# Optimization experiments

Hardware: AMD Instinct MI355X
Metric: run time of the kernel (lower is better)

The kernel has to match this reference:

```python
import jax, jax.numpy as jnp
import numpy as np

B = 16384
D1 = 256
D2 = 256
D_FF = 1024
N_BINS = 16
TAIL = 3.0
MIN_VAL = 1e-3
MIN_TOTAL = N_BINS * MIN_VAL
TAIL_CONST = float(np.log(np.exp(1.0 - MIN_VAL) - 1.0))
D_OUT = (3 * N_BINS - 1) * D2  # 12032


def setup_inputs() -> dict:
    key = jax.random.key(0)
    ks = jax.random.split(key, 8)
    s = lambda fan: 1.0 / np.sqrt(fan)
    return {
        'x1': jax.random.normal(ks[0], (B, D1), jnp.float32),
        'x2': jax.random.normal(ks[1], (B, D2), jnp.float32),
        'W0': jax.random.normal(ks[2], (D1, D_FF), jnp.float32) * s(D1),
        'b0': jnp.zeros((D_FF,), jnp.float32),
        'W1': jax.random.normal(ks[3], (D_FF, D_FF), jnp.float32) * s(D_FF),
        'b1': jnp.zeros((D_FF,), jnp.float32),
        'W2': jax.random.normal(ks[4], (D_FF, D_OUT), jnp.float32) * s(D_FF),
        'b2': jnp.zeros((D_OUT,), jnp.float32),
    }


def _rqs_forward(x, wu, hu, du):
    # x: [B, D2]; wu, hu: [B, D2, N_BINS]; du: [B, D2, N_BINS-1]
    widths = MIN_VAL + (1.0 - MIN_TOTAL) * jax.nn.softmax(wu, axis=-1)
    heights = MIN_VAL + (1.0 - MIN_TOTAL) * jax.nn.softmax(hu, axis=-1)
    cw = jnp.cumsum(widths, axis=-1)
    cw = jnp.concatenate([jnp.zeros_like(cw[..., :1]), cw], axis=-1)
    cw = 2.0 * TAIL * cw - TAIL  # x bin edges in [-TAIL, TAIL], [B,D2,N_BINS+1]
    ch = jnp.cumsum(heights, axis=-1)
    ch = jnp.concatenate([jnp.zeros_like(ch[..., :1]), ch], axis=-1)
    ch = 2.0 * TAIL * ch - TAIL  # y bin edges
    w = cw[..., 1:] - cw[..., :-1]
    h = ch[..., 1:] - ch[..., :-1]
    # boundary derivatives padded so softplus(TAIL_CONST)+MIN_VAL == 1 (linear tails)
    pad = jnp.full_like(du[..., :1], TAIL_CONST)
    d = MIN_VAL + jax.nn.softplus(jnp.concatenate([pad, du, pad], axis=-1))  # [B,D2,N_BINS+1]
    inside = (x > -TAIL) & (x < TAIL)
    xc = jnp.clip(x, -TAIL, TAIL)
    # data-dependent bin search against interior edges
    idx = jnp.sum((xc[..., None] >= cw[..., 1:-1]).astype(jnp.int32), axis=-1)  # [B,D2]
    take = lambda a: jnp.take_along_axis(a, idx[..., None], axis=-1)[..., 0]
    xk = take(cw[..., :-1]); yk = take(ch[..., :-1])
    wk = take(w); hk = take(h)
    dk = take(d[..., :-1]); dk1 = take(d[..., 1:])
    sk = hk / wk
    theta = (xc - xk) / wk
    t1m = theta * (1.0 - theta)
    denom = sk + (dk + dk1 - 2.0 * sk) * t1m
    y = yk + hk * (sk * theta * theta + dk * t1m) / denom
    deriv = sk * sk * (dk1 * theta * theta + 2.0 * sk * t1m + dk * (1.0 - theta) ** 2) / (denom * denom)
    y = jnp.where(inside, y, x)            # identity tails
    logdet = jnp.where(inside, jnp.log(deriv), 0.0)
    return y, jnp.sum(logdet, axis=-1)     # [B,D2], [B]


def reference(x1, x2, W0, b0, W1, b1, W2, b2):
    # conditioner MLP: x1 -> spline parameters
    hdn = jax.nn.relu(x1 @ W0 + b0)
    hdn = jax.nn.relu(hdn @ W1 + b1)
    p = (hdn @ W2 + b2).reshape(-1, D2, 3 * N_BINS - 1)
    wu = p[..., :N_BINS]
    hu = p[..., N_BINS:2 * N_BINS]
    du = p[..., 2 * N_BINS:]
    y2, logdet = _rqs_forward(x2, wu, hu, du)
    return y2, logdet
```

## Files before the change

### kernel.cpp

```cpp
#include <hip/hip_runtime.h>
#include <math.h>

using u16 = unsigned short;
using bf16x8 = __attribute__((ext_vector_type(8))) short;
using f32x4  = __attribute__((ext_vector_type(4))) float;

#define DEV static __device__ __forceinline__

DEV u16 f2bf(float f) {
  union { float f; unsigned u; } v; v.f = f;
  unsigned u = v.u + 0x7fffu + ((v.u >> 16) & 1u);
  return (u16)(u >> 16);
}

DEV void gload16(const void* g, void* l) {
  __builtin_amdgcn_global_load_lds(
      (const __attribute__((address_space(1))) void*)g,
      (__attribute__((address_space(3))) void*)l, 16, 0, 0);
}

__global__ void k_conv_bf16(const float* __restrict__ in, u16* __restrict__ out, int n) {
  int i = blockIdx.x * 256 + threadIdx.x;
  if (i < n) out[i] = f2bf(in[i]);
}

__global__ void k_transconv(const float* __restrict__ in, u16* __restrict__ out,
                            int K, int Nin, int Nout, int pack) {
  __shared__ float t[32][33];
  int kb = blockIdx.x * 32, nb = blockIdx.y * 32;
  int tx = threadIdx.x & 31, ty = threadIdx.x >> 5;
  #pragma unroll
  for (int i = 0; i < 4; ++i) {
    int k = kb + ty + i * 8;
    int no = nb + tx;
    float v = 0.f;
    if (k < K && no < Nout) {
      if (pack) {
        int r = no % 48;
        if (r < 47) v = in[(size_t)k * Nin + (no / 48) * 47 + r];
      } else {
        v = in[(size_t)k * Nin + no];
      }
    }
    t[ty + i * 8][tx] = v;
  }
  __syncthreads();
  #pragma unroll
  for (int i = 0; i < 4; ++i) {
    int no = nb + ty + i * 8;
    int k = kb + tx;
    if (no < Nout && k < K) out[(size_t)no * K + k] = f2bf(t[tx][ty + i * 8]);
  }
}

__global__ __launch_bounds__(256)
void k_gemm_relu(const u16* __restrict__ A, const u16* __restrict__ Bt,
                 const float* __restrict__ bias, u16* __restrict__ C,
                 int N, int K) {
  constexpr int BM = 128, BN = 128, BK = 32;
  __shared__ __align__(16) u16 lds[(BM + BN) * BK];
  int tid = threadIdx.x, w = tid >> 6, lane = tid & 63;
  int bn = blockIdx.x, bm = blockIdx.y;
  int brow = bm * BM, bcol = bn * BN;
  int wm = w >> 1, wn = w & 1;
  int fr = lane & 15, fg = lane >> 4;
  f32x4 acc[4][4];
  #pragma unroll
  for (int i = 0; i < 4; ++i)
    #pragma unroll
    for (int j = 0; j < 4; ++j) acc[i][j] = (f32x4){0.f, 0.f, 0.f, 0.f};

  constexpr int ACH = BM * BK / 8;
  constexpr int CALLS = (BM + BN) * BK / 8 / 64;

  for (int kt = 0; kt < K; kt += BK) {
    for (int j = 0; j * 4 + w < CALLS; ++j) {
      int cb = (j * 4 + w) * 64;
      int c = cb + lane;
      const u16* g;
      if (c < ACH) {
        int row = c >> 2, c8 = c & 3;
        g = A + (size_t)(brow + row) * K + kt + c8 * 8;
      } else {
        int b = c - ACH;
        int nn = b >> 2, c8 = b & 3;
        g = Bt + (size_t)(bcol + nn) * K + kt + c8 * 8;
      }
      gload16(g, &lds[cb * 8]);
    }
    asm volatile("s_waitcnt vmcnt(0)" ::: "memory");
    __syncthreads();

    const u16* Al = lds;
    const u16* Bl = lds + BM * BK;
    bf16x8 af[4], bfr[4];
    #pragma unroll
    for (int mi = 0; mi < 4; ++mi)
      af[mi] = *(const bf16x8*)&Al[(wm * 64 + mi * 16 + fr) * BK + fg * 8];
    #pragma unroll
    for (int ni = 0; ni < 4; ++ni)
      bfr[ni] = *(const bf16x8*)&Bl[(wn * 64 + ni * 16 + fr) * BK + fg * 8];
    #pragma unroll
    for (int mi = 0; mi < 4; ++mi)
      #pragma unroll
      for (int ni = 0; ni < 4; ++ni)
        acc[mi][ni] = __builtin_amdgcn_mfma_f32_16x16x32_bf16(af[mi], bfr[ni], acc[mi][ni], 0, 0, 0);
    __syncthreads();
  }

  #pragma unroll
  for (int ni = 0; ni < 4; ++ni) {
    int col = bcol + wn * 64 + ni * 16 + fr;
    float bb = bias[col];
    #pragma unroll
    for (int mi = 0; mi < 4; ++mi) {
      #pragma unroll
      for (int q = 0; q < 4; ++q) {
        int row = brow + wm * 64 + mi * 16 + fg * 4 + q;
        float vv = acc[mi][ni][q] + bb;
        C[(size_t)row * N + col] = f2bf(vv > 0.f ? vv : 0.f);
      }
    }
  }
}

__global__ __launch_bounds__(256, 2)
void k_gemm3_fused(const u16* __restrict__ A, const u16* __restrict__ Bt,
                   const float* __restrict__ b2, const float* __restrict__ x2,
                   float* __restrict__ y2, float* __restrict__ ldpart) {
  extern __shared__ char smem[];
  const int tid = threadIdx.x, w = tid >> 6, lane = tid & 63;
  const int fr = lane & 15, fg = lane >> 4;

  const int bid = blockIdx.x;
  const int bm = bid >> 6;
  const int bn = ((bid & 7) << 3) | ((bid >> 3) & 7);
  const int brow = bm * 256;

  const int csrc = (tid & 7) ^ ((tid >> 3) & 7);
  const u16* gB[6];
  #pragma unroll
  for (int k = 0; k < 6; ++k)
    gB[k] = Bt + (size_t)(bn * 192 + (tid >> 3) + 32 * k) * 1024 + csrc * 8;

#define ISSUE_B(t1) {                                                 \
    const size_t ko_ = (size_t)(t1) * 64;                             \
    char* pb_ = smem + ((t1) & 1) * 24576;                            \
    gload16(gB[0] + ko_, pb_ + tid * 16);                             \
    gload16(gB[1] + ko_, pb_ + tid * 16 + 4096);                      \
    gload16(gB[2] + ko_, pb_ + tid * 16 + 8192);                      \
    gload16(gB[3] + ko_, pb_ + tid * 16 + 12288);                     \
    gload16(gB[4] + ko_, pb_ + tid * 16 + 16384);                     \
    gload16(gB[5] + ko_, pb_ + tid * 16 + 20480); }

  const u16* gAm[4];
  #pragma unroll
  for (int m = 0; m < 4; ++m)
    gAm[m] = A + (size_t)(brow + w * 64 + m * 16 + fr) * 1024 + fg * 8;

  const int sc0 = ((fg ^ (fr & 7)) << 4);
  const int sc1 = (((4 + fg) ^ (fr & 7)) << 4);

  f32x4 acc[4][12];
  #pragma unroll
  for (int m = 0; m < 4; ++m)
    #pragma unroll
    for (int n = 0; n < 12; ++n) acc[m][n] = (f32x4){0.f, 0.f, 0.f, 0.f};

  bf16x8 a[4][2];

  ISSUE_B(0);
  #pragma unroll
  for (int m = 0; m < 4; ++m) {
    a[m][0] = *(const bf16x8*)(gAm[m]);
    a[m][1] = *(const bf16x8*)(gAm[m] + 32);
  }
  asm volatile("s_waitcnt vmcnt(0)" ::: "memory");
  __syncthreads();

  for (int t = 0; t < 16; ++t) {
    if (t < 15) ISSUE_B(t + 1);
    const char* Bb = smem + (t & 1) * 24576;
    __builtin_amdgcn_s_setprio(1);
    #pragma unroll
    for (int kk = 0; kk < 2; ++kk) {
      const int sc = kk ? sc1 : sc0;
      #pragma unroll
      for (int n = 0; n < 12; ++n) {
        bf16x8 b = *(const bf16x8*)(Bb + (n * 16 + fr) * 128 + sc);
        #pragma unroll
        for (int m = 0; m < 4; ++m)
          acc[m][n] = __builtin_amdgcn_mfma_f32_16x16x32_bf16(a[m][kk], b, acc[m][n], 0, 0, 0);
      }
    }
    __builtin_amdgcn_s_setprio(0);
    if (t < 15) {
      const size_t ko = (size_t)(t + 1) * 64;
      #pragma unroll
      for (int m = 0; m < 4; ++m) {
        a[m][0] = *(const bf16x8*)(gAm[m] + ko);
        a[m][1] = *(const bf16x8*)(gAm[m] + ko + 32);
      }
      asm volatile("s_waitcnt vmcnt(0)" ::: "memory");
      __syncthreads();
    }
  }
  __syncthreads();

  float* slot = (float*)smem;
  float* ldacc = (float*)(smem + 50176);
  #pragma unroll
  for (int g = 0; g < 4; ++g) {
    #pragma unroll
    for (int m = 0; m < 4; ++m)
      #pragma unroll
      for (int j = 0; j < 3; ++j) {
        const int n = g * 3 + j;
        #pragma unroll
        for (int q = 0; q < 4; ++q)
          slot[(w * 64 + m * 16 + fg * 4 + q) * 49 + j * 16 + fr] = acc[m][n][q];
      }
    __syncthreads();
    {
      const int r = tid;
      const float* pr = slot + r * 49;
      const int grow = brow + r;
      const int d2 = bn * 4 + g;
      const float* bb = b2 + (size_t)d2 * 47;

      float wv[16], hv[16];
      #pragma unroll
      for (int j = 0; j < 16; ++j) wv[j] = pr[j] + bb[j];
      #pragma unroll
      for (int j = 0; j < 16; ++j) hv[j] = pr[16 + j] + bb[16 + j];

      float x = x2[(size_t)grow * 256 + d2];
      float xc = fminf(fmaxf(x, -3.f), 3.f);

      float mw = wv[0];
      #pragma unroll
      for (int j = 1; j < 16; ++j) mw = fmaxf(mw, wv[j]);
      float sw = 0.f;
      #pragma unroll
      for (int j = 0; j < 16; ++j) { wv[j] = __expf(wv[j] - mw); sw += wv[j]; }
      float scw = 0.984f / sw;

      float mh = hv[0];
      #pragma unroll
      for (int j = 1; j < 16; ++j) mh = fmaxf(mh, hv[j]);
      float sh = 0.f;
      #pragma unroll
      for (int j = 0; j < 16; ++j) { hv[j] = __expf(hv[j] - mh); sh += hv[j]; }
      float sch = 0.984f / sh;

      int idx = 0;
      float xk = -3.f, cum = 0.f;
      #pragma unroll
      for (int i = 1; i <= 15; ++i) {
        cum += 0.001f + wv[i - 1] * scw;
        float cwi = 6.f * cum - 3.f;
        if (xc >= cwi) { idx = i; xk = cwi; }
      }
      float yk = -3.f, cumh = 0.f;
      #pragma unroll
      for (int i = 1; i <= 15; ++i) {
        cumh += 0.001f + hv[i - 1] * sch;
        float chi = 6.f * cumh - 3.f;
        if (i == idx) yk = chi;
      }
      float wk = 1.f, hk = 1.f;
      #pragma unroll
      for (int i = 0; i < 16; ++i) {
        if (i == idx) {
          wk = 6.f * (0.001f + wv[i] * scw);
          hk = 6.f * (0.001f + hv[i] * sch);
        }
      }
      float dk = 1.f, dk1 = 1.f;
      #pragma unroll
      for (int i = 1; i <= 15; ++i) {
        float u = pr[32 + i - 1] + bb[32 + i - 1];
        float e = __expf(u);
        float dd = 0.001f + (u > 15.f ? u : log1pf(e));
        if (i == idx) dk = dd;
        if (i == idx + 1) dk1 = dd;
      }

      float sk = hk / wk;
      float th = (xc - xk) / wk;
      float om = 1.f - th;
      float t1m = th * om;
      float den = sk + (dk + dk1 - 2.f * sk) * t1m;
      float y = yk + hk * (sk * th * th + dk * t1m) / den;
      float deriv = sk * sk * (dk1 * th * th + 2.f * sk * t1m + dk * om * om) / (den * den);
      bool inside = (x > -3.f) && (x < 3.f);
      float yout = inside ? y : x;
      float ld = inside ? __logf(deriv) : 0.f;

      y2[(size_t)grow * 256 + d2] = yout;
      ldacc[r * 4 + g] = ld;
    }
    __syncthreads();
  }

  {
    float s = ldacc[tid * 4] + ldacc[tid * 4 + 1] + ldacc[tid * 4 + 2] + ldacc[tid * 4 + 3];
    ldpart[(size_t)bn * 16384 + brow + tid] = s;
  }
}

__global__ void k_reduce_ld(const float* __restrict__ part, float* __restrict__ out) {
  int r = blockIdx.x * 256 + threadIdx.x;
  float s = 0.f;
  for (int j = 0; j < 64; ++j) s += part[(size_t)j * 16384 + r];
  out[r] = s;
}

extern "C" void kernel_launch(void* const* d_in, const int* in_sizes, int n_in,
                              void* d_out, int out_size, void* d_ws, size_t ws_size,
                              hipStream_t stream) {
  const float* x1 = (const float*)d_in[0];
  const float* x2 = (const float*)d_in[1];
  const float* W0 = (const float*)d_in[2];
  const float* b0 = (const float*)d_in[3];
  const float* W1 = (const float*)d_in[4];
  const float* b1 = (const float*)d_in[5];
  const float* W2 = (const float*)d_in[6];
  const float* b2 = (const float*)d_in[7];
  float* y2 = (float*)d_out;
  float* logdet = y2 + (size_t)16384 * 256;

  char* ws = (char*)d_ws;
  u16* W2t = (u16*)ws;
  u16* W0t = (u16*)(ws + 25165824);
  u16* W1t = (u16*)(ws + 25165824 + 524288);
  u16* x1b = (u16*)(ws + 27787264);
  float* ldp = (float*)(ws + 27787264);
  u16* h1  = (u16*)(ws + 36175872);
  u16* h2  = (u16*)(ws + 69730304);

  hipFuncSetAttribute((const void*)k_gemm3_fused,
                      hipFuncAttributeMaxDynamicSharedMemorySize, 54272);

  k_conv_bf16<<<16384, 256, 0, stream>>>(x1, x1b, 16384 * 256);
  k_transconv<<<dim3(8, 32), 256, 0, stream>>>(W0, W0t, 256, 1024, 1024, 0);
  k_transconv<<<dim3(32, 32), 256, 0, stream>>>(W1, W1t, 1024, 1024, 1024, 0);
  k_transconv<<<dim3(32, 384), 256, 0, stream>>>(W2, W2t, 1024, 12032, 12288, 1);

  k_gemm_relu<<<dim3(8, 128), 256, 0, stream>>>(x1b, W0t, b0, h1, 1024, 256);
  k_gemm_relu<<<dim3(8, 128), 256, 0, stream>>>(h1, W1t, b1, h2, 1024, 1024);
  k_gemm3_fused<<<4096, 256, 54272, stream>>>(h2, W2t, b2, x2, y2, ldp);
  k_reduce_ld<<<64, 256, 0, stream>>>(ldp, logdet);
}
```

Measured before the change: 752.4 us.

## Halve gemm3 row tile to raise occupancy and split A-load waits

The fused final GEMM now uses a 128-row tile instead of 256, which halves the accumulator registers per thread and doubles the grid. Launch bounds go up to 4 blocks per CU and shared memory drops slightly. The k-loop is split into two half-steps so the A-fragment reloads overlap the MFMAs, with a partial vmcnt wait and a bare barrier replacing the full wait plus syncthreads. The epilogue processes two d2 columns per pass and writes twice as many logdet partials, which the reduce kernel now sums over 128 slices. The cost is that each B tile is reused across fewer rows, so global and LDS traffic for B roughly doubles.

Measured after the change: 741.8 us. No clear change (-1.4%).

```diff
diff --git a/kernel.cpp b/kernel.cpp
--- a/kernel.cpp
+++ b/kernel.cpp
@@ -124,7 +124,7 @@
   }
 }
 
-__global__ __launch_bounds__(256, 2)
+__global__ __launch_bounds__(256, 4)
 void k_gemm3_fused(const u16* __restrict__ A, const u16* __restrict__ Bt,
                    const float* __restrict__ b2, const float* __restrict__ x2,
                    float* __restrict__ y2, float* __restrict__ ldpart) {
@@ -135,97 +135,95 @@
   const int bid = blockIdx.x;
   const int bm = bid >> 6;
   const int bn = ((bid & 7) << 3) | ((bid >> 3) & 7);
-  const int brow = bm * 256;
+  const int brow = bm * 128;
 
   const int csrc = (tid & 7) ^ ((tid >> 3) & 7);
-  const u16* gB[6];
-  #pragma unroll
-  for (int k = 0; k < 6; ++k)
-    gB[k] = Bt + (size_t)(bn * 192 + (tid >> 3) + 32 * k) * 1024 + csrc * 8;
+  const u16* gB0 = Bt + (size_t)(bn * 192 + (tid >> 3)) * 1024 + csrc * 8;
 
 #define ISSUE_B(t1) {                                                 \
     const size_t ko_ = (size_t)(t1) * 64;                             \
-    char* pb_ = smem + ((t1) & 1) * 24576;                            \
-    gload16(gB[0] + ko_, pb_ + tid * 16);                             \
-    gload16(gB[1] + ko_, pb_ + tid * 16 + 4096);                      \
-    gload16(gB[2] + ko_, pb_ + tid * 16 + 8192);                      \
-    gload16(gB[3] + ko_, pb_ + tid * 16 + 12288);                     \
-    gload16(gB[4] + ko_, pb_ + tid * 16 + 16384);                     \
-    gload16(gB[5] + ko_, pb_ + tid * 16 + 20480); }
-
-  const u16* gAm[4];
-  #pragma unroll
-  for (int m = 0; m < 4; ++m)
-    gAm[m] = A + (size_t)(brow + w * 64 + m * 16 + fr) * 1024 + fg * 8;
+    char* pb_ = smem + ((t1) & 1) * 24576 + tid * 16;                 \
+    gload16(gB0 + ko_, pb_);                                          \
+    gload16(gB0 + 32768 + ko_, pb_ + 4096);                           \
+    gload16(gB0 + 65536 + ko_, pb_ + 8192);                           \
+    gload16(gB0 + 98304 + ko_, pb_ + 12288);                          \
+    gload16(gB0 + 131072 + ko_, pb_ + 16384);                         \
+    gload16(gB0 + 163840 + ko_, pb_ + 20480); }
+
+  const u16* gA0 = A + (size_t)(brow + w * 32 + fr) * 1024 + fg * 8;
 
   const int sc0 = ((fg ^ (fr & 7)) << 4);
   const int sc1 = (((4 + fg) ^ (fr & 7)) << 4);
 
-  f32x4 acc[4][12];
-  #pragma unroll
-  for (int m = 0; m < 4; ++m)
+  f32x4 acc[2][12];
+  #pragma unroll
+  for (int m = 0; m < 2; ++m)
     #pragma unroll
     for (int n = 0; n < 12; ++n) acc[m][n] = (f32x4){0.f, 0.f, 0.f, 0.f};
 
-  bf16x8 a[4][2];
+  bf16x8 a[2][2];
 
   ISSUE_B(0);
-  #pragma unroll
-  for (int m = 0; m < 4; ++m) {
-    a[m][0] = *(const bf16x8*)(gAm[m]);
-    a[m][1] = *(const bf16x8*)(gAm[m] + 32);
-  }
+  a[0][0] = *(const bf16x8*)(gA0);
+  a[0][1] = *(const bf16x8*)(gA0 + 32);
+  a[1][0] = *(const bf16x8*)(gA0 + 16384);
+  a[1][1] = *(const bf16x8*)(gA0 + 16384 + 32);
   asm volatile("s_waitcnt vmcnt(0)" ::: "memory");
   __syncthreads();
 
   for (int t = 0; t < 16; ++t) {
     if (t < 15) ISSUE_B(t + 1);
     const char* Bb = smem + (t & 1) * 24576;
+    const size_t ko = (size_t)(t + 1) * 64;
     __builtin_amdgcn_s_setprio(1);
     #pragma unroll
-    for (int kk = 0; kk < 2; ++kk) {
-      const int sc = kk ? sc1 : sc0;
-      #pragma unroll
-      for (int n = 0; n < 12; ++n) {
-        bf16x8 b = *(const bf16x8*)(Bb + (n * 16 + fr) * 128 + sc);
-        #pragma unroll
-        for (int m = 0; m < 4; ++m)
-          acc[m][n] = __builtin_amdgcn_mfma_f32_16x16x32_bf16(a[m][kk], b, acc[m][n], 0, 0, 0);
-      }
+    for (int n = 0; n < 12; ++n) {
+      bf16x8 b = *(const bf16x8*)(Bb + (n * 16 + fr) * 128 + sc0);
+      acc[0][n] = __builtin_amdgcn_mfma_f32_16x16x32_bf16(a[0][0], b, acc[0][n], 0, 0, 0);
+      acc[1][n] = __builtin_amdgcn_mfma_f32_16x16x32_bf16(a[1][0], b, acc[1][n], 0, 0, 0);
     }
     __builtin_amdgcn_s_setprio(0);
     if (t < 15) {
-      const size_t ko = (size_t)(t + 1) * 64;
-      #pragma unroll
-      for (int m = 0; m < 4; ++m) {
-        a[m][0] = *(const bf16x8*)(gAm[m] + ko);
-        a[m][1] = *(const bf16x8*)(gAm[m] + ko + 32);
-      }
-      asm volatile("s_waitcnt vmcnt(0)" ::: "memory");
-      __syncthreads();
-    }
-  }
-  __syncthreads();
-
-  float* slot = (float*)smem;
-  float* ldacc = (float*)(smem + 50176);
-  #pragma unroll
-  for (int g = 0; g < 4; ++g) {
-    #pragma unroll
-    for (int m = 0; m < 4; ++m)
-      #pragma unroll
-      for (int j = 0; j < 3; ++j) {
-        const int n = g * 3 + j;
+      a[0][0] = *(const bf16x8*)(gA0 + ko);
+      a[1][0] = *(const bf16x8*)(gA0 + 16384 + ko);
+    }
+    __builtin_amdgcn_s_setprio(1);
+    #pragma unroll
+    for (int n = 0; n < 12; ++n) {
+      bf16x8 b = *(const bf16x8*)(Bb + (n * 16 + fr) * 128 + sc1);
+      acc[0][n] = __builtin_amdgcn_mfma_f32_16x16x32_bf16(a[0][1], b, acc[0][n], 0, 0, 0);
+      acc[1][n] = __builtin_amdgcn_mfma_f32_16x16x32_bf16(a[1][1], b, acc[1][n], 0, 0, 0);
+    }
+    __builtin_amdgcn_s_setprio(0);
+    if (t < 15) {
+      a[0][1] = *(const bf16x8*)(gA0 + ko + 32);
+      a[1][1] = *(const bf16x8*)(gA0 + 16384 + ko + 32);
+      asm volatile("s_waitcnt vmcnt(4)" ::: "memory");
+    }
+    __builtin_amdgcn_s_barrier();
+  }
+
+  float* slotf = (float*)smem;
+  const int h = tid >> 7, rrow = tid & 127;
+  float ldsum = 0.f;
+  #pragma unroll
+  for (int r = 0; r < 2; ++r) {
+    #pragma unroll
+    for (int hh = 0; hh < 2; ++hh)
+      #pragma unroll
+      for (int m = 0; m < 2; ++m)
         #pragma unroll
-        for (int q = 0; q < 4; ++q)
-          slot[(w * 64 + m * 16 + fg * 4 + q) * 49 + j * 16 + fr] = acc[m][n][q];
-      }
+        for (int j = 0; j < 3; ++j) {
+          const int n = (r * 2 + hh) * 3 + j;
+          #pragma unroll
+          for (int q = 0; q < 4; ++q)
+            slotf[hh * 6272 + (w * 32 + m * 16 + fg * 4 + q) * 49 + j * 16 + fr] = acc[m][n][q];
+        }
     __syncthreads();
     {
-      const int r = tid;
-      const float* pr = slot + r * 49;
-      const int grow = brow + r;
-      const int d2 = bn * 4 + g;
+      const float* pr = slotf + h * 6272 + rrow * 49;
+      const int grow = brow + rrow;
+      const int d2 = bn * 4 + r * 2 + h;
       const float* bb = b2 + (size_t)d2 * 47;
 
       float wv[16], hv[16];
@@ -298,21 +296,18 @@
       float ld = inside ? __logf(deriv) : 0.f;
 
       y2[(size_t)grow * 256 + d2] = yout;
-      ldacc[r * 4 + g] = ld;
+      ldsum += ld;
     }
     __syncthreads();
   }
 
-  {
-    float s = ldacc[tid * 4] + ldacc[tid * 4 + 1] + ldacc[tid * 4 + 2] + ldacc[tid * 4 + 3];
-    ldpart[(size_t)bn * 16384 + brow + tid] = s;
-  }
+  ldpart[(size_t)(bn * 2 + h) * 16384 + brow + rrow] = ldsum;
 }
 
 __global__ void k_reduce_ld(const float* __restrict__ part, float* __restrict__ out) {
   int r = blockIdx.x * 256 + threadIdx.x;
   float s = 0.f;
-  for (int j = 0; j < 64; ++j) s += part[(size_t)j * 16384 + r];
+  for (int j = 0; j < 128; ++j) s += part[(size_t)j * 16384 + r];
   out[r] = s;
 }
 
@@ -340,7 +335,7 @@
   u16* h2  = (u16*)(ws + 69730304);
 
   hipFuncSetAttribute((const void*)k_gemm3_fused,
-                      hipFuncAttributeMaxDynamicSharedMemorySize, 54272);
+                      hipFuncAttributeMaxDynamicSharedMemorySize, 50176);
 
   k_conv_bf16<<<16384, 256, 0, stream>>>(x1, x1b, 16384 * 256);
   k_transconv<<<dim3(8, 32), 256, 0, stream>>>(W0, W0t, 256, 1024, 1024, 0);
@@ -349,6 +344,6 @@
 
   k_gemm_relu<<<dim3(8, 128), 256, 0, stream>>>(x1b, W0t, b0, h1, 1024, 256);
   k_gemm_relu<<<dim3(8, 128), 256, 0, stream>>>(h1, W1t, b1, h2, 1024, 1024);
-  k_gemm3_fused<<<4096, 256, 54272, stream>>>(h2, W2t, b2, x2, y2, ldp);
+  k_gemm3_fused<<<8192, 256, 50176, stream>>>(h2, W2t, b2, x2, y2, ldp);
   k_reduce_ld<<<64, 256, 0, stream>>>(ldp, logdet);
 }
```
